# Optimization experiments

Hardware: AMD Instinct MI355X
Metric: run time of the kernel (lower is better)

## Reference

```python
import jax, jax.numpy as jnp
import numpy as np
import math

D_MODEL = 1024
N_HEADS = 16
GEOM_DIM = 7
B, S = 4, 1024


def setup_inputs() -> dict:
    key = jax.random.key(0)
    ks = jax.random.split(key, 12)
    w = lambda k, shape: (jax.random.normal(k, shape, dtype=jnp.float32) * 0.02)
    return {
        "x": jax.random.normal(ks[0], (B, S, D_MODEL), dtype=jnp.float32),
        "geom_feat": jax.random.normal(ks[1], (B, S, S, GEOM_DIM), dtype=jnp.float32),
        "mask": jax.random.randint(ks[2], (B, S), 0, 2, dtype=jnp.int32),
        "Wq": w(ks[3], (D_MODEL, D_MODEL)), "bq": jnp.zeros((D_MODEL,), jnp.float32),
        "Wk": w(ks[4], (D_MODEL, D_MODEL)), "bk": jnp.zeros((D_MODEL,), jnp.float32),
        "Wv": w(ks[5], (D_MODEL, D_MODEL)), "bv": jnp.zeros((D_MODEL,), jnp.float32),
        "Wo": w(ks[6], (D_MODEL, D_MODEL)), "bo": jnp.zeros((D_MODEL,), jnp.float32),
        "Wg": w(ks[7], (GEOM_DIM, N_HEADS)), "bg": jnp.zeros((N_HEADS,), jnp.float32),
    }


def reference(x, geom_feat, mask, Wq, bq, Wk, bk, Wv, bv, Wo, bo, Wg, bg):
    b, s, d = x.shape
    h = Wg.shape[1]
    dk = d // h
    scale = math.sqrt(dk)
    # QKV projections -> [b, h, s, dk]
    Q = (x @ Wq + bq).reshape(b, s, h, dk).transpose(0, 2, 1, 3)
    K = (x @ Wk + bk).reshape(b, s, h, dk).transpose(0, 2, 1, 3)
    V = (x @ Wv + bv).reshape(b, s, h, dk).transpose(0, 2, 1, 3)
    # attention scores [b, h, s, s]
    scores = jnp.einsum("bhqd,bhkd->bhqk", Q, K) / scale
    # geometric structure bias: [b,s,s,geom_dim] -> [b,s,s,h] -> [b,h,s,s]
    struct_bias = (geom_feat @ Wg + bg).transpose(0, 3, 1, 2)
    scores = scores + struct_bias
    # key-padding mask [b, s] -> [b, 1, 1, s]
    scores = jnp.where(mask[:, None, None, :] == 0, -10000.0, scores)
    attn = jax.nn.softmax(scores, axis=-1)  # dropout disabled (eval / p=0)
    ctx = jnp.einsum("bhqk,bhkd->bhqd", attn, V)
    ctx = ctx.transpose(0, 2, 1, 3).reshape(b, s, d)
    return ctx @ Wo + bo
```

## Files before the change

### kernel.cpp

```cpp
#include <hip/hip_runtime.h>
#include <hip/hip_bf16.h>
#include <math.h>

#define BB 4
#define SS 1024
#define DD 1024
#define NH 16
#define DK 64
#define GD 7

typedef _Float16 half8 __attribute__((ext_vector_type(8)));
typedef _Float16 half4v __attribute__((ext_vector_type(4)));
typedef float floatx4 __attribute__((ext_vector_type(4)));

__device__ __forceinline__ void async_cp16(const void* g, void* l) {
  __builtin_amdgcn_global_load_lds(
      (const __attribute__((address_space(1))) void*)g,
      (__attribute__((address_space(3))) void*)l, 16, 0, 0);
}

__device__ inline half8 cvt8(const float4 a, const float4 b) {
  half8 h;
  h[0] = (_Float16)a.x; h[1] = (_Float16)a.y; h[2] = (_Float16)a.z; h[3] = (_Float16)a.w;
  h[4] = (_Float16)b.x; h[5] = (_Float16)b.y; h[6] = (_Float16)b.z; h[7] = (_Float16)b.w;
  return h;
}

__global__ __launch_bounds__(256) void prep(const float* __restrict__ x,
                                            _Float16* __restrict__ xh,
                                            const float* __restrict__ Wq,
                                            const float* __restrict__ Wk,
                                            const float* __restrict__ Wv,
                                            const float* __restrict__ Wo,
                                            _Float16* __restrict__ Wt) {
  __shared__ _Float16 Tl[64 * 72];
  const int t = threadIdx.x;
  if (blockIdx.x < 2048) {
    const int i = blockIdx.x * 256 + t;
    const float4 a = ((const float4*)x)[i * 2];
    const float4 b = ((const float4*)x)[i * 2 + 1];
    ((half8*)xh)[i] = cvt8(a, b);
    return;
  }
  const int pf = blockIdx.x - 2048;
  const int z = pf >> 8, rem = pf & 255;
  const int n0 = (rem >> 4) * 64, k0 = (rem & 15) * 64;
  const float* src = (z == 0) ? Wq : (z == 1) ? Wk : (z == 2) ? Wv : Wo;
#pragma unroll
  for (int i = 0; i < 4; ++i) {
    const int u = i * 256 + t;
    const int r = u >> 4, c4 = (u & 15) * 4;
    const float4 v = *(const float4*)(src + (size_t)(k0 + r) * DD + n0 + c4);
    Tl[(c4 + 0) * 72 + r] = (_Float16)v.x;
    Tl[(c4 + 1) * 72 + r] = (_Float16)v.y;
    Tl[(c4 + 2) * 72 + r] = (_Float16)v.z;
    Tl[(c4 + 3) * 72 + r] = (_Float16)v.w;
  }
  __syncthreads();
  _Float16* dst = Wt + (size_t)z * DD * DD;
#pragma unroll
  for (int i = 0; i < 2; ++i) {
    const int u = i * 256 + t;
    const int nr = u >> 3, ks = u & 7;
    const half8 hv = *(const half8*)&Tl[nr * 72 + ks * 8];
    *(half8*)(dst + (size_t)(n0 + nr) * DD + k0 + ks * 8) = hv;
  }
}

template <bool PRE>
__global__ __launch_bounds__(256) void fused0(const _Float16* __restrict__ A,
                                              const _Float16* __restrict__ Bt,
                                              const float* __restrict__ bq,
                                              const float* __restrict__ bk,
                                              const float* __restrict__ bv,
                                              _Float16* __restrict__ Oq,
                                              _Float16* __restrict__ Ok,
                                              _Float16* __restrict__ Ov,
                                              const float* __restrict__ geom,
                                              const int* __restrict__ mask,
                                              const float* __restrict__ Wg,
                                              const float* __restrict__ bg,
                                              unsigned char* __restrict__ bias8) {
  const int t = threadIdx.x;
  int role, idx;
  if (PRE) {
    const int g = blockIdx.x, grp = g / 11, rem = g % 11;
    if (rem < 3) { role = 0; idx = grp * 3 + rem; }
    else         { role = 1; idx = grp * 8 + rem - 3; }
  } else {
    role = 0; idx = blockIdx.x;
  }

  if (role == 0) {
    __shared__ _Float16 Als[128 * 64];
    __shared__ _Float16 Bls[128 * 64];
    const int w = t >> 6, lane = t & 63, quad = lane >> 4, col = lane & 15;
    const int m0 = (idx & 31) * 128, n0 = (idx >> 5) * 128;
    const int mw = (w >> 1) * 64, nw = (w & 1) * 64;
    const int lr = lane >> 3, ls = lane & 7;
    const int swz8 = (ls ^ lr) * 8;
    const floatx4 zero4 = {0.f, 0.f, 0.f, 0.f};
    floatx4 acc[4][4];
#pragma unroll
    for (int i = 0; i < 4; ++i)
#pragma unroll
      for (int j = 0; j < 4; ++j) acc[i][j] = zero4;

    const _Float16* aBase = A + (size_t)(m0 + lr) * DD + swz8;
    const _Float16* bBase = Bt + (size_t)(n0 + lr) * DD + swz8;

    for (int k0 = 0; k0 < DD; k0 += 64) {
#pragma unroll
      for (int it = 0; it < 4; ++it) {
        const int rb = it * 32 + w * 8;
        async_cp16(aBase + (size_t)rb * DD + k0, &Als[rb * 64]);
        async_cp16(bBase + (size_t)rb * DD + k0, &Bls[rb * 64]);
      }
      __syncthreads();
#pragma unroll
      for (int kk = 0; kk < 2; ++kk) {
        half8 af[4], bf[4];
        const int sz = ((quad + kk * 4) ^ (col & 7)) * 8;
#pragma unroll
        for (int i = 0; i < 4; ++i)
          af[i] = *(const half8*)&Als[(mw + i * 16 + col) * 64 + sz];
#pragma unroll
        for (int j = 0; j < 4; ++j)
          bf[j] = *(const half8*)&Bls[(nw + j * 16 + col) * 64 + sz];
#pragma unroll
        for (int i = 0; i < 4; ++i)
#pragma unroll
          for (int j = 0; j < 4; ++j)
            acc[i][j] =
                __builtin_amdgcn_mfma_f32_16x16x32_f16(af[i], bf[j], acc[i][j], 0, 0, 0);
      }
      __syncthreads();
    }

#pragma unroll
    for (int j = 0; j < 4; ++j) {
      const int n = n0 + nw + j * 16 + col;
      const int which = n >> 10, hd = n & 1023;
      const int h = hd >> 6, d = hd & 63;
      const float* bp = (which == 0) ? bq : (which == 1) ? bk : bv;
      const float bias = bp[hd];
      _Float16* ob = (which == 0) ? Oq : (which == 1) ? Ok : Ov;
#pragma unroll
      for (int i = 0; i < 4; ++i) {
#pragma unroll
        for (int reg = 0; reg < 4; ++reg) {
          const int m = m0 + mw + i * 16 + quad * 4 + reg;
          const int b = m >> 10, s = m & 1023;
          ob[(((size_t)b * NH + h) * SS + s) * DK + d] = (_Float16)(acc[i][j][reg] + bias);
        }
      }
    }
    return;
  }

  if constexpr (PRE) {
    __shared__ float wgL[GD * NH + NH];
    const int r = idx;
    const int b = r >> 9;
    const int q = (r & 511) * 2 + (t >> 7);
    const int k8 = (t & 127) * 8;
    if (t < GD * NH) wgL[t] = Wg[t];
    if (t < NH) wgL[GD * NH + t] = bg[t];

    const float* gp = geom + ((size_t)b * SS + q) * SS * GD + (size_t)k8 * GD;
    float4 gv[14];
#pragma unroll
    for (int i = 0; i < 14; ++i) gv[i] = *(const float4*)(gp + i * 4);
    const float* gf = (const float*)gv;

    const int4 m4a = *(const int4*)(mask + b * SS + k8);
    const int4 m4b = *(const int4*)(mask + b * SS + k8 + 4);
    const int mk[8] = {m4a.x, m4a.y, m4a.z, m4a.w, m4b.x, m4b.y, m4b.z, m4b.w};

    __syncthreads();

    unsigned char* dst = bias8 + ((size_t)b * NH * SS + q) * SS + k8;
#pragma unroll
    for (int h = 0; h < NH; ++h) {
      float wg[GD];
#pragma unroll
      for (int g = 0; g < GD; ++g) wg[g] = wgL[g * NH + h];
      const float bgh = wgL[GD * NH + h];
      float bi[8];
#pragma unroll
      for (int k2 = 0; k2 < 8; ++k2) {
        float s = bgh;
#pragma unroll
        for (int g = 0; g < GD; ++g) s = fmaf(gf[k2 * GD + g], wg[g], s);
        bi[k2] = mk[k2] ? s : -100.f;
      }
      int w0 = 0, w1 = 0;
      w0 = __builtin_amdgcn_cvt_pk_fp8_f32(bi[0], bi[1], w0, false);
      w0 = __builtin_amdgcn_cvt_pk_fp8_f32(bi[2], bi[3], w0, true);
      w1 = __builtin_amdgcn_cvt_pk_fp8_f32(bi[4], bi[5], w1, false);
      w1 = __builtin_amdgcn_cvt_pk_fp8_f32(bi[6], bi[7], w1, true);
      uint2 u2v;
      u2v.x = (unsigned)w0;
      u2v.y = (unsigned)w1;
      *(uint2*)(dst + (size_t)h * SS * SS) = u2v;
    }
  }
}

__global__ __launch_bounds__(256) void hgemm1(const _Float16* __restrict__ A,
                                              const _Float16* __restrict__ Bt,
                                              const float* __restrict__ b0,
                                              float* __restrict__ Of) {
  __shared__ _Float16 Als[128 * 64];
  __shared__ _Float16 Bls[128 * 64];
  const int t = threadIdx.x;
  const int w = t >> 6, lane = t & 63, quad = lane >> 4, col = lane & 15;
  const int m0 = blockIdx.x * 128, n0 = blockIdx.y * 128;
  const int mw = (w >> 1) * 64, nw = (w & 1) * 64;
  const int lr = lane >> 3, ls = lane & 7;
  const int swz8 = (ls ^ lr) * 8;
  const floatx4 zero4 = {0.f, 0.f, 0.f, 0.f};
  floatx4 acc[4][4];
#pragma unroll
  for (int i = 0; i < 4; ++i)
#pragma unroll
    for (int j = 0; j < 4; ++j) acc[i][j] = zero4;

  const _Float16* aBase = A + (size_t)(m0 + lr) * DD + swz8;
  const _Float16* bBase = Bt + (size_t)(n0 + lr) * DD + swz8;

  for (int k0 = 0; k0 < DD; k0 += 64) {
#pragma unroll
    for (int it = 0; it < 4; ++it) {
      const int rb = it * 32 + w * 8;
      async_cp16(aBase + (size_t)rb * DD + k0, &Als[rb * 64]);
      async_cp16(bBase + (size_t)rb * DD + k0, &Bls[rb * 64]);
    }
    __syncthreads();
#pragma unroll
    for (int kk = 0; kk < 2; ++kk) {
      half8 af[4], bf[4];
      const int sz = ((quad + kk * 4) ^ (col & 7)) * 8;
#pragma unroll
      for (int i = 0; i < 4; ++i) af[i] = *(const half8*)&Als[(mw + i * 16 + col) * 64 + sz];
#pragma unroll
      for (int j = 0; j < 4; ++j) bf[j] = *(const half8*)&Bls[(nw + j * 16 + col) * 64 + sz];
#pragma unroll
      for (int i = 0; i < 4; ++i)
#pragma unroll
        for (int j = 0; j < 4; ++j)
          acc[i][j] = __builtin_amdgcn_mfma_f32_16x16x32_f16(af[i], bf[j], acc[i][j], 0, 0, 0);
    }
    __syncthreads();
  }

#pragma unroll
  for (int j = 0; j < 4; ++j) {
    const int n = n0 + nw + j * 16 + col;
    const float bias = b0[n];
#pragma unroll
    for (int i = 0; i < 4; ++i) {
#pragma unroll
      for (int reg = 0; reg < 4; ++reg) {
        const int m = m0 + mw + i * 16 + quad * 4 + reg;
        Of[(size_t)m * DD + n] = acc[i][j][reg] + bias;
      }
    }
  }
}

template <bool PREBIAS>
__global__ __launch_bounds__(256) void attn(const _Float16* __restrict__ Q,
                                            const _Float16* __restrict__ K,
                                            const _Float16* __restrict__ V,
                                            const unsigned char* __restrict__ bias8,
                                            const float* __restrict__ geom,
                                            const int* __restrict__ mask,
                                            const float* __restrict__ Wg,
                                            const float* __restrict__ bg,
                                            _Float16* __restrict__ ctxbuf) {
  __shared__ _Float16 Ks[64 * 64];
  __shared__ _Float16 Vt[64 * 72];
  __shared__ unsigned char biasL[PREBIAS ? 64 * 80 : 64 * 144];
  __shared__ unsigned char mskL[SS];

  const int t = threadIdx.x;
  const int w = t >> 6, lane = t & 63, quad = lane >> 4, col = lane & 15;
  const int h = blockIdx.x, qt = blockIdx.y, b = blockIdx.z;
  const int q0 = qt * 64;
  const size_t bh = (size_t)b * NH + h;
  const _Float16* Qb = Q + bh * SS * DK;
  const _Float16* Kb = K + bh * SS * DK;
  const _Float16* Vb = V + bh * SS * DK;
  _Float16* biasLf = (_Float16*)biasL;

  const int lr = lane >> 3, ls = lane & 7;
  const int swz8 = (ls ^ lr) * 8;

  {
#pragma unroll
    for (int it = 0; it < 2; ++it) {
      const int rb = it * 32 + w * 8;
      async_cp16(Qb + (size_t)(q0 + rb + lr) * DK + swz8, &Ks[rb * 64]);
    }
  }
  if constexpr (!PREBIAS) {
    const int4 m4 = *(const int4*)(mask + b * SS + t * 4);
    mskL[t * 4 + 0] = m4.x != 0;
    mskL[t * 4 + 1] = m4.y != 0;
    mskL[t * 4 + 2] = m4.z != 0;
    mskL[t * 4 + 3] = m4.w != 0;
  }
  __syncthreads();
  half8 qfrag[2];
  {
    const int qrow = w * 16 + col;
#pragma unroll
    for (int kk = 0; kk < 2; ++kk)
      qfrag[kk] = *(const half8*)&Ks[qrow * 64 + (((quad + kk * 4) ^ (col & 7)) * 8)];
  }

  float wgv[GD];
  float bgh = 0.f;
  const float* gptr = nullptr;
  if constexpr (!PREBIAS) {
#pragma unroll
    for (int g = 0; g < GD; ++g) wgv[g] = Wg[g * NH + h];
    bgh = bg[h];
    gptr = geom + (((size_t)b * SS + (q0 + (t >> 2))) * SS + (t & 3) * 16) * GD;
  }
  const unsigned char* bb8 = nullptr;
  if constexpr (PREBIAS) bb8 = bias8 + (bh * SS + q0) * SS;

  const floatx4 zero4 = {0.f, 0.f, 0.f, 0.f};
  floatx4 ctx[4] = {zero4, zero4, zero4, zero4};
  float lsum = 0.f;

  const int kg = (t >> 4) * 4, dg = (t & 15) * 4;
  const int cg = (kg & 0x20) | ((kg & 0x0C) << 1) | ((kg & 0x10) >> 2);

  for (int c = 0; c < 16; ++c) {
    const int k0c = c * 64;
    __syncthreads();

    {
#pragma unroll
      for (int it = 0; it < 2; ++it) {
        const int rb = it * 32 + w * 8;
        async_cp16(Kb + (size_t)(k0c + rb + lr) * DK + swz8, &Ks[rb * 64]);
      }
    }
    {
      half4v f[4];
#pragma unroll
      for (int e = 0; e < 4; ++e)
        f[e] = *(const half4v*)(Vb + (size_t)(k0c + kg + e) * DK + dg);
#pragma unroll
      for (int i = 0; i < 4; ++i) {
        half4v hv = {f[0][i], f[1][i], f[2][i], f[3][i]};
        *(half4v*)&Vt[(dg + i) * 72 + cg] = hv;
      }
    }
    if constexpr (PREBIAS) {
      const int row = t >> 2, seg = (t & 3) * 16;
      const uint4 v = *(const uint4*)(bb8 + (size_t)row * SS + k0c + seg);
      *(uint4*)&biasL[row * 80 + seg] = v;
    } else {
      const int gq = t >> 2, gk = (t & 3) * 16;
#pragma unroll
      for (int sg = 0; sg < 4; ++sg) {
        float4 gvv[7];
#pragma unroll
        for (int i7 = 0; i7 < 7; ++i7) gvv[i7] = *(const float4*)(gptr + sg * 28 + i7 * 4);
        const float* gf = (const float*)gvv;
        half4v bv;
#pragma unroll
        for (int k2 = 0; k2 < 4; ++k2) {
          float bi = bgh;
#pragma unroll
          for (int g = 0; g < GD; ++g) bi = fmaf(gf[k2 * GD + g], wgv[g], bi);
          bv[k2] = mskL[k0c + gk + sg * 4 + k2] ? (_Float16)bi : (_Float16)(-100.f);
        }
        *(half4v*)&biasLf[gq * 72 + gk + sg * 4] = bv;
      }
      gptr += 64 * GD;
    }
    __syncthreads();

    floatx4 sc[4] = {zero4, zero4, zero4, zero4};
#pragma unroll
    for (int nt = 0; nt < 4; ++nt) {
      const int key = nt * 16 + col;
#pragma unroll
      for (int kk = 0; kk < 2; ++kk) {
        const half8 kf = *(const half8*)&Ks[key * 64 + (((quad + kk * 4) ^ (col & 7)) * 8)];
        sc[nt] = __builtin_amdgcn_mfma_f32_16x16x32_f16(kf, qfrag[kk], sc[nt], 0, 0, 0);
      }
    }

    float ps[4][4];
#pragma unroll
    for (int nt = 0; nt < 4; ++nt) {
      float bias4[4];
      if constexpr (PREBIAS) {
        const unsigned bw =
            *(const unsigned*)&biasL[(w * 16 + col) * 80 + nt * 16 + quad * 4];
        bias4[0] = __builtin_amdgcn_cvt_f32_fp8((int)bw, 0);
        bias4[1] = __builtin_amdgcn_cvt_f32_fp8((int)bw, 1);
        bias4[2] = __builtin_amdgcn_cvt_f32_fp8((int)bw, 2);
        bias4[3] = __builtin_amdgcn_cvt_f32_fp8((int)bw, 3);
      } else {
#pragma unroll
        for (int reg = 0; reg < 4; ++reg)
          bias4[reg] = (float)biasLf[(w * 16 + col) * 72 + nt * 16 + quad * 4 + reg];
      }
#pragma unroll
      for (int reg = 0; reg < 4; ++reg) {
        const float s = fmaf(sc[nt][reg], 0.125f, bias4[reg]);
        const float p = __expf(s);
        lsum += p;
        ps[nt][reg] = p;
      }
    }

#pragma unroll
    for (int kk = 0; kk < 2; ++kk) {
      half8 pf;
      pf[0] = (_Float16)ps[2 * kk][0];
      pf[1] = (_Float16)ps[2 * kk][1];
      pf[2] = (_Float16)ps[2 * kk][2];
      pf[3] = (_Float16)ps[2 * kk][3];
      pf[4] = (_Float16)ps[2 * kk + 1][0];
      pf[5] = (_Float16)ps[2 * kk + 1][1];
      pf[6] = (_Float16)ps[2 * kk + 1][2];
      pf[7] = (_Float16)ps[2 * kk + 1][3];
#pragma unroll
      for (int nt = 0; nt < 4; ++nt) {
        const half8 vb = *(const half8*)&Vt[(nt * 16 + col) * 72 + quad * 8 + kk * 32];
        ctx[nt] = __builtin_amdgcn_mfma_f32_16x16x32_f16(vb, pf, ctx[nt], 0, 0, 0);
      }
    }
  }

  float l = lsum;
  l += __shfl_xor(l, 16, 64);
  l += __shfl_xor(l, 32, 64);
  const float inv = 1.f / l;

  _Float16* op = ctxbuf + ((size_t)b * SS + q0 + w * 16 + col) * DD + h * DK + quad * 4;
#pragma unroll
  for (int nt = 0; nt < 4; ++nt) {
    half4v o;
#pragma unroll
    for (int reg = 0; reg < 4; ++reg) o[reg] = (_Float16)(ctx[nt][reg] * inv);
    *(half4v*)(op + nt * 16) = o;
  }
}

extern "C" void kernel_launch(void* const* d_in, const int* in_sizes, int n_in,
                              void* d_out, int out_size, void* d_ws, size_t ws_size,
                              hipStream_t stream) {
  const float* x    = (const float*)d_in[0];
  const float* geom = (const float*)d_in[1];
  const int*   mask = (const int*)d_in[2];
  const float* Wq   = (const float*)d_in[3];
  const float* bq   = (const float*)d_in[4];
  const float* Wk   = (const float*)d_in[5];
  const float* bk   = (const float*)d_in[6];
  const float* Wv   = (const float*)d_in[7];
  const float* bv   = (const float*)d_in[8];
  const float* Wo   = (const float*)d_in[9];
  const float* bo   = (const float*)d_in[10];
  const float* Wg   = (const float*)d_in[11];
  const float* bg   = (const float*)d_in[12];
  float* out = (float*)d_out;

  const size_t NEL = (size_t)BB * SS * DD;
  char* p = (char*)d_ws;
  _Float16* xh   = (_Float16*)p;            p += NEL * 2;
  _Float16* Wt   = (_Float16*)p;            p += NEL * 2;
  _Float16* Qh   = (_Float16*)p;            p += NEL * 2;
  _Float16* Kh   = (_Float16*)p;            p += NEL * 2;
  _Float16* Vh   = (_Float16*)p;            p += NEL * 2;
  _Float16* ctxh = (_Float16*)p;            p += NEL * 2;
  unsigned char* bias8 = (unsigned char*)p;
  const size_t need = (size_t)48 * 1024 * 1024 + (size_t)BB * NH * SS * SS;
  const bool prebias = ws_size >= need;

  prep<<<3072, 256, 0, stream>>>(x, xh, Wq, Wk, Wv, Wo, Wt);

  if (prebias) {
    fused0<true><<<2816, 256, 0, stream>>>(xh, Wt, bq, bk, bv, Qh, Kh, Vh,
                                           geom, mask, Wg, bg, bias8);
    attn<true><<<dim3(NH, SS / 64, BB), 256, 0, stream>>>(Qh, Kh, Vh, bias8, geom, mask,
                                                          Wg, bg, ctxh);
  } else {
    fused0<false><<<768, 256, 0, stream>>>(xh, Wt, bq, bk, bv, Qh, Kh, Vh,
                                           geom, mask, Wg, bg, nullptr);
    attn<false><<<dim3(NH, SS / 64, BB), 256, 0, stream>>>(Qh, Kh, Vh, nullptr, geom, mask,
                                                           Wg, bg, ctxh);
  }

  hgemm1<<<dim3(32, 8), 256, 0, stream>>>(ctxh, Wt + (size_t)3 * DD * DD, bo, out);
}
```

Before: 322.5 us.

## Split fused QKV/bias kernel and software-pipeline K/V/bias loads in attention

Result: slower. 332.2 us (+3.0%).

```diff
diff --git a/kernel.cpp b/kernel.cpp
--- a/kernel.cpp
+++ b/kernel.cpp
@@ -67,143 +67,132 @@
   }
 }
 
-template <bool PRE>
-__global__ __launch_bounds__(256) void fused0(const _Float16* __restrict__ A,
-                                              const _Float16* __restrict__ Bt,
-                                              const float* __restrict__ bq,
-                                              const float* __restrict__ bk,
-                                              const float* __restrict__ bv,
-                                              _Float16* __restrict__ Oq,
-                                              _Float16* __restrict__ Ok,
-                                              _Float16* __restrict__ Ov,
-                                              const float* __restrict__ geom,
-                                              const int* __restrict__ mask,
-                                              const float* __restrict__ Wg,
-                                              const float* __restrict__ bg,
-                                              unsigned char* __restrict__ bias8) {
+__global__ __launch_bounds__(256) void gemmQKV(const _Float16* __restrict__ A,
+                                               const _Float16* __restrict__ Bt,
+                                               const float* __restrict__ bq,
+                                               const float* __restrict__ bk,
+                                               const float* __restrict__ bv,
+                                               _Float16* __restrict__ Oq,
+                                               _Float16* __restrict__ Ok,
+                                               _Float16* __restrict__ Ov) {
+  __shared__ _Float16 Als[128 * 64];
+  __shared__ _Float16 Bls[128 * 64];
   const int t = threadIdx.x;
-  int role, idx;
-  if (PRE) {
-    const int g = blockIdx.x, grp = g / 11, rem = g % 11;
-    if (rem < 3) { role = 0; idx = grp * 3 + rem; }
-    else         { role = 1; idx = grp * 8 + rem - 3; }
-  } else {
-    role = 0; idx = blockIdx.x;
-  }
-
-  if (role == 0) {
-    __shared__ _Float16 Als[128 * 64];
-    __shared__ _Float16 Bls[128 * 64];
-    const int w = t >> 6, lane = t & 63, quad = lane >> 4, col = lane & 15;
-    const int m0 = (idx & 31) * 128, n0 = (idx >> 5) * 128;
-    const int mw = (w >> 1) * 64, nw = (w & 1) * 64;
-    const int lr = lane >> 3, ls = lane & 7;
-    const int swz8 = (ls ^ lr) * 8;
-    const floatx4 zero4 = {0.f, 0.f, 0.f, 0.f};
-    floatx4 acc[4][4];
-#pragma unroll
-    for (int i = 0; i < 4; ++i)
-#pragma unroll
-      for (int j = 0; j < 4; ++j) acc[i][j] = zero4;
-
-    const _Float16* aBase = A + (size_t)(m0 + lr) * DD + swz8;
-    const _Float16* bBase = Bt + (size_t)(n0 + lr) * DD + swz8;
-
-    for (int k0 = 0; k0 < DD; k0 += 64) {
-#pragma unroll
-      for (int it = 0; it < 4; ++it) {
-        const int rb = it * 32 + w * 8;
-        async_cp16(aBase + (size_t)rb * DD + k0, &Als[rb * 64]);
-        async_cp16(bBase + (size_t)rb * DD + k0, &Bls[rb * 64]);
-      }
-      __syncthreads();
-#pragma unroll
-      for (int kk = 0; kk < 2; ++kk) {
-        half8 af[4], bf[4];
-        const int sz = ((quad + kk * 4) ^ (col & 7)) * 8;
-#pragma unroll
-        for (int i = 0; i < 4; ++i)
-          af[i] = *(const half8*)&Als[(mw + i * 16 + col) * 64 + sz];
+  const int raw = blockIdx.x;
+  const int idx = (raw & 7) * 96 + (raw >> 3);
+  const int w = t >> 6, lane = t & 63, quad = lane >> 4, col = lane & 15;
+  const int m0 = (idx & 31) * 128, n0 = (idx >> 5) * 128;
+  const int mw = (w >> 1) * 64, nw = (w & 1) * 64;
+  const int lr = lane >> 3, ls = lane & 7;
+  const int swz8 = (ls ^ lr) * 8;
+  const floatx4 zero4 = {0.f, 0.f, 0.f, 0.f};
+  floatx4 acc[4][4];
+#pragma unroll
+  for (int i = 0; i < 4; ++i)
+#pragma unroll
+    for (int j = 0; j < 4; ++j) acc[i][j] = zero4;
+
+  const _Float16* aBase = A + (size_t)(m0 + lr) * DD + swz8;
+  const _Float16* bBase = Bt + (size_t)(n0 + lr) * DD + swz8;
+
+  for (int k0 = 0; k0 < DD; k0 += 64) {
+#pragma unroll
+    for (int it = 0; it < 4; ++it) {
+      const int rb = it * 32 + w * 8;
+      async_cp16(aBase + (size_t)rb * DD + k0, &Als[rb * 64]);
+      async_cp16(bBase + (size_t)rb * DD + k0, &Bls[rb * 64]);
+    }
+    __syncthreads();
+#pragma unroll
+    for (int kk = 0; kk < 2; ++kk) {
+      half8 af[4], bf[4];
+      const int sz = ((quad + kk * 4) ^ (col & 7)) * 8;
+#pragma unroll
+      for (int i = 0; i < 4; ++i)
+        af[i] = *(const half8*)&Als[(mw + i * 16 + col) * 64 + sz];
+#pragma unroll
+      for (int j = 0; j < 4; ++j)
+        bf[j] = *(const half8*)&Bls[(nw + j * 16 + col) * 64 + sz];
+#pragma unroll
+      for (int i = 0; i < 4; ++i)
 #pragma unroll
         for (int j = 0; j < 4; ++j)
-          bf[j] = *(const half8*)&Bls[(nw + j * 16 + col) * 64 + sz];
-#pragma unroll
-        for (int i = 0; i < 4; ++i)
-#pragma unroll
-          for (int j = 0; j < 4; ++j)
-            acc[i][j] =
-                __builtin_amdgcn_mfma_f32_16x16x32_f16(af[i], bf[j], acc[i][j], 0, 0, 0);
-      }
-      __syncthreads();
-    }
-
-#pragma unroll
-    for (int j = 0; j < 4; ++j) {
-      const int n = n0 + nw + j * 16 + col;
-      const int which = n >> 10, hd = n & 1023;
-      const int h = hd >> 6, d = hd & 63;
-      const float* bp = (which == 0) ? bq : (which == 1) ? bk : bv;
-      const float bias = bp[hd];
-      _Float16* ob = (which == 0) ? Oq : (which == 1) ? Ok : Ov;
-#pragma unroll
-      for (int i = 0; i < 4; ++i) {
-#pragma unroll
-        for (int reg = 0; reg < 4; ++reg) {
-          const int m = m0 + mw + i * 16 + quad * 4 + reg;
-          const int b = m >> 10, s = m & 1023;
-          ob[(((size_t)b * NH + h) * SS + s) * DK + d] = (_Float16)(acc[i][j][reg] + bias);
-        }
-      }
-    }
-    return;
-  }
-
-  if constexpr (PRE) {
-    __shared__ float wgL[GD * NH + NH];
-    const int r = idx;
-    const int b = r >> 9;
-    const int q = (r & 511) * 2 + (t >> 7);
-    const int k8 = (t & 127) * 8;
-    if (t < GD * NH) wgL[t] = Wg[t];
-    if (t < NH) wgL[GD * NH + t] = bg[t];
-
-    const float* gp = geom + ((size_t)b * SS + q) * SS * GD + (size_t)k8 * GD;
-    float4 gv[14];
-#pragma unroll
-    for (int i = 0; i < 14; ++i) gv[i] = *(const float4*)(gp + i * 4);
-    const float* gf = (const float*)gv;
-
-    const int4 m4a = *(const int4*)(mask + b * SS + k8);
-    const int4 m4b = *(const int4*)(mask + b * SS + k8 + 4);
-    const int mk[8] = {m4a.x, m4a.y, m4a.z, m4a.w, m4b.x, m4b.y, m4b.z, m4b.w};
-
+          acc[i][j] =
+              __builtin_amdgcn_mfma_f32_16x16x32_f16(af[i], bf[j], acc[i][j], 0, 0, 0);
+    }
     __syncthreads();
-
-    unsigned char* dst = bias8 + ((size_t)b * NH * SS + q) * SS + k8;
-#pragma unroll
-    for (int h = 0; h < NH; ++h) {
-      float wg[GD];
-#pragma unroll
-      for (int g = 0; g < GD; ++g) wg[g] = wgL[g * NH + h];
-      const float bgh = wgL[GD * NH + h];
-      float bi[8];
-#pragma unroll
-      for (int k2 = 0; k2 < 8; ++k2) {
-        float s = bgh;
-#pragma unroll
-        for (int g = 0; g < GD; ++g) s = fmaf(gf[k2 * GD + g], wg[g], s);
-        bi[k2] = mk[k2] ? s : -100.f;
-      }
-      int w0 = 0, w1 = 0;
-      w0 = __builtin_amdgcn_cvt_pk_fp8_f32(bi[0], bi[1], w0, false);
-      w0 = __builtin_amdgcn_cvt_pk_fp8_f32(bi[2], bi[3], w0, true);
-      w1 = __builtin_amdgcn_cvt_pk_fp8_f32(bi[4], bi[5], w1, false);
-      w1 = __builtin_amdgcn_cvt_pk_fp8_f32(bi[6], bi[7], w1, true);
-      uint2 u2v;
-      u2v.x = (unsigned)w0;
-      u2v.y = (unsigned)w1;
-      *(uint2*)(dst + (size_t)h * SS * SS) = u2v;
-    }
+  }
+
+#pragma unroll
+  for (int j = 0; j < 4; ++j) {
+    const int n = n0 + nw + j * 16 + col;
+    const int which = n >> 10, hd = n & 1023;
+    const int h = hd >> 6, d = hd & 63;
+    const float* bp = (which == 0) ? bq : (which == 1) ? bk : bv;
+    const float bias = bp[hd];
+    _Float16* ob = (which == 0) ? Oq : (which == 1) ? Ok : Ov;
+#pragma unroll
+    for (int i = 0; i < 4; ++i) {
+#pragma unroll
+      for (int reg = 0; reg < 4; ++reg) {
+        const int m = m0 + mw + i * 16 + quad * 4 + reg;
+        const int b = m >> 10, s = m & 1023;
+        ob[(((size_t)b * NH + h) * SS + s) * DK + d] = (_Float16)(acc[i][j][reg] + bias);
+      }
+    }
+  }
+}
+
+__global__ __launch_bounds__(256) void biasprep(const float* __restrict__ geom,
+                                                const int* __restrict__ mask,
+                                                const float* __restrict__ Wg,
+                                                const float* __restrict__ bg,
+                                                unsigned char* __restrict__ bias8) {
+  __shared__ float wgL[GD * NH + NH];
+  const int t = threadIdx.x;
+  const int r = blockIdx.x;
+  const int b = r >> 9;
+  const int q = (r & 511) * 2 + (t >> 7);
+  const int k8 = (t & 127) * 8;
+  if (t < GD * NH) wgL[t] = Wg[t];
+  if (t < NH) wgL[GD * NH + t] = bg[t];
+
+  const float* gp = geom + ((size_t)b * SS + q) * SS * GD + (size_t)k8 * GD;
+  float4 gv[14];
+#pragma unroll
+  for (int i = 0; i < 14; ++i) gv[i] = *(const float4*)(gp + i * 4);
+  const float* gf = (const float*)gv;
+
+  const int4 m4a = *(const int4*)(mask + b * SS + k8);
+  const int4 m4b = *(const int4*)(mask + b * SS + k8 + 4);
+  const int mk[8] = {m4a.x, m4a.y, m4a.z, m4a.w, m4b.x, m4b.y, m4b.z, m4b.w};
+
+  __syncthreads();
+
+  unsigned char* dst = bias8 + ((size_t)b * NH * SS + q) * SS + k8;
+#pragma unroll
+  for (int h = 0; h < NH; ++h) {
+    float wg[GD];
+#pragma unroll
+    for (int g = 0; g < GD; ++g) wg[g] = wgL[g * NH + h];
+    const float bgh = wgL[GD * NH + h];
+    float bi[8];
+#pragma unroll
+    for (int k2 = 0; k2 < 8; ++k2) {
+      float s = bgh;
+#pragma unroll
+      for (int g = 0; g < GD; ++g) s = fmaf(gf[k2 * GD + g], wg[g], s);
+      bi[k2] = mk[k2] ? s : -100.f;
+    }
+    int w0 = 0, w1 = 0;
+    w0 = __builtin_amdgcn_cvt_pk_fp8_f32(bi[0], bi[1], w0, false);
+    w0 = __builtin_amdgcn_cvt_pk_fp8_f32(bi[2], bi[3], w0, true);
+    w1 = __builtin_amdgcn_cvt_pk_fp8_f32(bi[4], bi[5], w1, false);
+    w1 = __builtin_amdgcn_cvt_pk_fp8_f32(bi[6], bi[7], w1, true);
+    uint2 u2v;
+    u2v.x = (unsigned)w0;
+    u2v.y = (unsigned)w1;
+    *(uint2*)(dst + (size_t)h * SS * SS) = u2v;
   }
 }
 
@@ -269,20 +258,15 @@
   }
 }
 
-template <bool PREBIAS>
-__global__ __launch_bounds__(256) void attn(const _Float16* __restrict__ Q,
-                                            const _Float16* __restrict__ K,
-                                            const _Float16* __restrict__ V,
-                                            const unsigned char* __restrict__ bias8,
-                                            const float* __restrict__ geom,
-                                            const int* __restrict__ mask,
-                                            const float* __restrict__ Wg,
-                                            const float* __restrict__ bg,
-                                            _Float16* __restrict__ ctxbuf) {
-  __shared__ _Float16 Ks[64 * 64];
+__global__ __launch_bounds__(256) void attnP(const _Float16* __restrict__ Q,
+                                             const _Float16* __restrict__ K,
+                                             const _Float16* __restrict__ V,
+                                             const unsigned char* __restrict__ bias8,
+                                             _Float16* __restrict__ ctxbuf) {
+  __shared__ _Float16 Qs[64 * 64];
+  __shared__ _Float16 Ks[2][64 * 64];
   __shared__ _Float16 Vt[64 * 72];
-  __shared__ unsigned char biasL[PREBIAS ? 64 * 80 : 64 * 144];
-  __shared__ unsigned char mskL[SS];
+  __shared__ unsigned char biasL[64 * 80];
 
   const int t = threadIdx.x;
   const int w = t >> 6, lane = t & 63, quad = lane >> 4, col = lane & 15;
@@ -292,19 +276,172 @@
   const _Float16* Qb = Q + bh * SS * DK;
   const _Float16* Kb = K + bh * SS * DK;
   const _Float16* Vb = V + bh * SS * DK;
-  _Float16* biasLf = (_Float16*)biasL;
+  const unsigned char* bb8 = bias8 + (bh * SS + q0) * SS;
 
   const int lr = lane >> 3, ls = lane & 7;
   const int swz8 = (ls ^ lr) * 8;
 
+  const int kg = (t >> 4) * 4, dg = (t & 15) * 4;
+  const int cg = (kg & 0x20) | ((kg & 0x0C) << 1) | ((kg & 0x10) >> 2);
+  const int brow = t >> 2, bseg = (t & 3) * 16;
+
+#pragma unroll
+  for (int it = 0; it < 2; ++it) {
+    const int rb = it * 32 + w * 8;
+    async_cp16(Qb + (size_t)(q0 + rb + lr) * DK + swz8, &Qs[rb * 64]);
+  }
+#pragma unroll
+  for (int it = 0; it < 2; ++it) {
+    const int rb = it * 32 + w * 8;
+    async_cp16(Kb + (size_t)(rb + lr) * DK + swz8, &Ks[0][rb * 64]);
+  }
+  half4v vreg[4];
+#pragma unroll
+  for (int e = 0; e < 4; ++e)
+    vreg[e] = *(const half4v*)(Vb + (size_t)(kg + e) * DK + dg);
+  uint4 breg = *(const uint4*)(bb8 + (size_t)brow * SS + bseg);
+
+  __syncthreads();
+  half8 qfrag[2];
   {
-#pragma unroll
-    for (int it = 0; it < 2; ++it) {
-      const int rb = it * 32 + w * 8;
-      async_cp16(Qb + (size_t)(q0 + rb + lr) * DK + swz8, &Ks[rb * 64]);
-    }
-  }
-  if constexpr (!PREBIAS) {
+    const int qrow = w * 16 + col;
+#pragma unroll
+    for (int kk = 0; kk < 2; ++kk)
+      qfrag[kk] = *(const half8*)&Qs[qrow * 64 + (((quad + kk * 4) ^ (col & 7)) * 8)];
+  }
+
+  const floatx4 zero4 = {0.f, 0.f, 0.f, 0.f};
+  floatx4 ctx[4] = {zero4, zero4, zero4, zero4};
+  float lsum = 0.f;
+
+  for (int c = 0; c < 16; ++c) {
+    const int cur = c & 1;
+    __syncthreads();
+
+    if (c < 15) {
+#pragma unroll
+      for (int it = 0; it < 2; ++it) {
+        const int rb = it * 32 + w * 8;
+        async_cp16(Kb + (size_t)((c + 1) * 64 + rb + lr) * DK + swz8,
+                   &Ks[cur ^ 1][rb * 64]);
+      }
+    }
+#pragma unroll
+    for (int i = 0; i < 4; ++i) {
+      half4v hv = {vreg[0][i], vreg[1][i], vreg[2][i], vreg[3][i]};
+      *(half4v*)&Vt[(dg + i) * 72 + cg] = hv;
+    }
+    *(uint4*)&biasL[brow * 80 + bseg] = breg;
+
+    asm volatile("s_waitcnt lgkmcnt(0)" ::: "memory");
+    __builtin_amdgcn_s_barrier();
+    __builtin_amdgcn_sched_barrier(0);
+
+    if (c < 15) {
+      const int kn = (c + 1) * 64;
+#pragma unroll
+      for (int e = 0; e < 4; ++e)
+        vreg[e] = *(const half4v*)(Vb + (size_t)(kn + kg + e) * DK + dg);
+      breg = *(const uint4*)(bb8 + (size_t)brow * SS + kn + bseg);
+    }
+    __builtin_amdgcn_sched_barrier(0);
+
+    floatx4 sc[4] = {zero4, zero4, zero4, zero4};
+#pragma unroll
+    for (int nt = 0; nt < 4; ++nt) {
+      const int key = nt * 16 + col;
+#pragma unroll
+      for (int kk = 0; kk < 2; ++kk) {
+        const half8 kf =
+            *(const half8*)&Ks[cur][key * 64 + (((quad + kk * 4) ^ (col & 7)) * 8)];
+        sc[nt] = __builtin_amdgcn_mfma_f32_16x16x32_f16(kf, qfrag[kk], sc[nt], 0, 0, 0);
+      }
+    }
+
+    float ps[4][4];
+#pragma unroll
+    for (int nt = 0; nt < 4; ++nt) {
+      const unsigned bw =
+          *(const unsigned*)&biasL[(w * 16 + col) * 80 + nt * 16 + quad * 4];
+      float bias4[4];
+      bias4[0] = __builtin_amdgcn_cvt_f32_fp8((int)bw, 0);
+      bias4[1] = __builtin_amdgcn_cvt_f32_fp8((int)bw, 1);
+      bias4[2] = __builtin_amdgcn_cvt_f32_fp8((int)bw, 2);
+      bias4[3] = __builtin_amdgcn_cvt_f32_fp8((int)bw, 3);
+#pragma unroll
+      for (int reg = 0; reg < 4; ++reg) {
+        const float s = fmaf(sc[nt][reg], 0.125f, bias4[reg]);
+        const float p = __expf(s);
+        lsum += p;
+        ps[nt][reg] = p;
+      }
+    }
+
+#pragma unroll
+    for (int kk = 0; kk < 2; ++kk) {
+      half8 pf;
+      pf[0] = (_Float16)ps[2 * kk][0];
+      pf[1] = (_Float16)ps[2 * kk][1];
+      pf[2] = (_Float16)ps[2 * kk][2];
+      pf[3] = (_Float16)ps[2 * kk][3];
+      pf[4] = (_Float16)ps[2 * kk + 1][0];
+      pf[5] = (_Float16)ps[2 * kk + 1][1];
+      pf[6] = (_Float16)ps[2 * kk + 1][2];
+      pf[7] = (_Float16)ps[2 * kk + 1][3];
+#pragma unroll
+      for (int nt = 0; nt < 4; ++nt) {
+        const half8 vb = *(const half8*)&Vt[(nt * 16 + col) * 72 + quad * 8 + kk * 32];
+        ctx[nt] = __builtin_amdgcn_mfma_f32_16x16x32_f16(vb, pf, ctx[nt], 0, 0, 0);
+      }
+    }
+  }
+
+  float l = lsum;
+  l += __shfl_xor(l, 16, 64);
+  l += __shfl_xor(l, 32, 64);
+  const float inv = 1.f / l;
+
+  _Float16* op = ctxbuf + ((size_t)b * SS + q0 + w * 16 + col) * DD + h * DK + quad * 4;
+#pragma unroll
+  for (int nt = 0; nt < 4; ++nt) {
+    half4v o;
+#pragma unroll
+    for (int reg = 0; reg < 4; ++reg) o[reg] = (_Float16)(ctx[nt][reg] * inv);
+    *(half4v*)(op + nt * 16) = o;
+  }
+}
+
+__global__ __launch_bounds__(256) void attnF(const _Float16* __restrict__ Q,
+                                             const _Float16* __restrict__ K,
+                                             const _Float16* __restrict__ V,
+                                             const float* __restrict__ geom,
+                                             const int* __restrict__ mask,
+                                             const float* __restrict__ Wg,
+                                             const float* __restrict__ bg,
+                                             _Float16* __restrict__ ctxbuf) {
+  __shared__ _Float16 Ks[64 * 64];
+  __shared__ _Float16 Vt[64 * 72];
+  __shared__ _Float16 biasLf[64 * 72];
+  __shared__ unsigned char mskL[SS];
+
+  const int t = threadIdx.x;
+  const int w = t >> 6, lane = t & 63, quad = lane >> 4, col = lane & 15;
+  const int h = blockIdx.x, qt = blockIdx.y, b = blockIdx.z;
+  const int q0 = qt * 64;
+  const size_t bh = (size_t)b * NH + h;
+  const _Float16* Qb = Q + bh * SS * DK;
+  const _Float16* Kb = K + bh * SS * DK;
+  const _Float16* Vb = V + bh * SS * DK;
+
+  const int lr = lane >> 3, ls = lane & 7;
+  const int swz8 = (ls ^ lr) * 8;
+
+#pragma unroll
+  for (int it = 0; it < 2; ++it) {
+    const int rb = it * 32 + w * 8;
+    async_cp16(Qb + (size_t)(q0 + rb + lr) * DK + swz8, &Ks[rb * 64]);
+  }
+  {
     const int4 m4 = *(const int4*)(mask + b * SS + t * 4);
     mskL[t * 4 + 0] = m4.x != 0;
     mskL[t * 4 + 1] = m4.y != 0;
@@ -321,16 +458,10 @@
   }
 
   float wgv[GD];
-  float bgh = 0.f;
-  const float* gptr = nullptr;
-  if constexpr (!PREBIAS) {
-#pragma unroll
-    for (int g = 0; g < GD; ++g) wgv[g] = Wg[g * NH + h];
-    bgh = bg[h];
-    gptr = geom + (((size_t)b * SS + (q0 + (t >> 2))) * SS + (t & 3) * 16) * GD;
-  }
-  const unsigned char* bb8 = nullptr;
-  if constexpr (PREBIAS) bb8 = bias8 + (bh * SS + q0) * SS;
+#pragma unroll
+  for (int g = 0; g < GD; ++g) wgv[g] = Wg[g * NH + h];
+  const float bgh = bg[h];
+  const float* gptr = geom + (((size_t)b * SS + (q0 + (t >> 2))) * SS + (t & 3) * 16) * GD;
 
   const floatx4 zero4 = {0.f, 0.f, 0.f, 0.f};
   floatx4 ctx[4] = {zero4, zero4, zero4, zero4};
@@ -343,12 +474,10 @@
     const int k0c = c * 64;
     __syncthreads();
 
-    {
-#pragma unroll
-      for (int it = 0; it < 2; ++it) {
-        const int rb = it * 32 + w * 8;
-        async_cp16(Kb + (size_t)(k0c + rb + lr) * DK + swz8, &Ks[rb * 64]);
-      }
+#pragma unroll
+    for (int it = 0; it < 2; ++it) {
+      const int rb = it * 32 + w * 8;
+      async_cp16(Kb + (size_t)(k0c + rb + lr) * DK + swz8, &Ks[rb * 64]);
     }
     {
       half4v f[4];
@@ -361,11 +490,7 @@
         *(half4v*)&Vt[(dg + i) * 72 + cg] = hv;
       }
     }
-    if constexpr (PREBIAS) {
-      const int row = t >> 2, seg = (t & 3) * 16;
-      const uint4 v = *(const uint4*)(bb8 + (size_t)row * SS + k0c + seg);
-      *(uint4*)&biasL[row * 80 + seg] = v;
-    } else {
+    {
       const int gq = t >> 2, gk = (t & 3) * 16;
 #pragma unroll
       for (int sg = 0; sg < 4; ++sg) {
@@ -401,22 +526,10 @@
     float ps[4][4];
 #pragma unroll
     for (int nt = 0; nt < 4; ++nt) {
-      float bias4[4];
-      if constexpr (PREBIAS) {
-        const unsigned bw =
-            *(const unsigned*)&biasL[(w * 16 + col) * 80 + nt * 16 + quad * 4];
-        bias4[0] = __builtin_amdgcn_cvt_f32_fp8((int)bw, 0);
-        bias4[1] = __builtin_amdgcn_cvt_f32_fp8((int)bw, 1);
-        bias4[2] = __builtin_amdgcn_cvt_f32_fp8((int)bw, 2);
-        bias4[3] = __builtin_amdgcn_cvt_f32_fp8((int)bw, 3);
-      } else {
-#pragma unroll
-        for (int reg = 0; reg < 4; ++reg)
-          bias4[reg] = (float)biasLf[(w * 16 + col) * 72 + nt * 16 + quad * 4 + reg];
-      }
 #pragma unroll
       for (int reg = 0; reg < 4; ++reg) {
-        const float s = fmaf(sc[nt][reg], 0.125f, bias4[reg]);
+        const float bias = (float)biasLf[(w * 16 + col) * 72 + nt * 16 + quad * 4 + reg];
+        const float s = fmaf(sc[nt][reg], 0.125f, bias);
         const float p = __expf(s);
         lsum += p;
         ps[nt][reg] = p;
@@ -488,17 +601,13 @@
   const bool prebias = ws_size >= need;
 
   prep<<<3072, 256, 0, stream>>>(x, xh, Wq, Wk, Wv, Wo, Wt);
+  gemmQKV<<<768, 256, 0, stream>>>(xh, Wt, bq, bk, bv, Qh, Kh, Vh);
 
   if (prebias) {
-    fused0<true><<<2816, 256, 0, stream>>>(xh, Wt, bq, bk, bv, Qh, Kh, Vh,
-                                           geom, mask, Wg, bg, bias8);
-    attn<true><<<dim3(NH, SS / 64, BB), 256, 0, stream>>>(Qh, Kh, Vh, bias8, geom, mask,
-                                                          Wg, bg, ctxh);
+    biasprep<<<2048, 256, 0, stream>>>(geom, mask, Wg, bg, bias8);
+    attnP<<<dim3(NH, SS / 64, BB), 256, 0, stream>>>(Qh, Kh, Vh, bias8, ctxh);
   } else {
-    fused0<false><<<768, 256, 0, stream>>>(xh, Wt, bq, bk, bv, Qh, Kh, Vh,
-                                           geom, mask, Wg, bg, nullptr);
-    attn<false><<<dim3(NH, SS / 64, BB), 256, 0, stream>>>(Qh, Kh, Vh, nullptr, geom, mask,
-                                                           Wg, bg, ctxh);
+    attnF<<<dim3(NH, SS / 64, BB), 256, 0, stream>>>(Qh, Kh, Vh, geom, mask, Wg, bg, ctxh);
   }
 
   hgemm1<<<dim3(32, 8), 256, 0, stream>>>(ctxh, Wt + (size_t)3 * DD * DD, bo, out);
```
